# Kernel optimization log

Hardware: AMD Instinct MI355X
Metric: run time of the kernel (lower is better)

## Reference

```python
import jax, jax.numpy as jnp
import numpy as np

COMMITMENT_COST = 0.25
NUM_EMBEDDINGS = 8192
EMBEDDING_DIM = 256
N_TOKENS = 32768


def setup_inputs() -> dict:
    key = jax.random.key(0)
    k1, k2 = jax.random.split(key)
    inputs = jax.random.normal(k1, (N_TOKENS, EMBEDDING_DIM), dtype=jnp.float32)
    embed = jax.random.normal(k2, (EMBEDDING_DIM, NUM_EMBEDDINGS), dtype=jnp.float32)
    return {"inputs": inputs, "embed": embed}


def reference(inputs, embed):
    # inputs: [N, D], embed: [D, K]
    input_shape = inputs.shape
    flat = inputs.reshape(-1, embed.shape[0])
    input_norm = jnp.sum(flat * flat, axis=1, keepdims=True)
    embed_norm = jnp.sum(embed * embed, axis=0, keepdims=True)
    distances = input_norm + embed_norm - 2.0 * (flat @ embed)
    encoding_indices = jnp.argmin(distances, axis=1)  # [N]
    # direct gather instead of one-hot matmul (same math)
    quantized = jnp.take(embed.T, encoding_indices, axis=0).reshape(input_shape)
    e_latent_loss = jnp.mean((jax.lax.stop_gradient(quantized) - inputs) ** 2)
    loss = COMMITMENT_COST * e_latent_loss
    # straight-through estimator
    quantized_st = inputs + jax.lax.stop_gradient(quantized - inputs)
    return quantized_st, loss, encoding_indices
```

## Files before the change

### kernel.cpp

```cpp
#include <hip/hip_runtime.h>

#define N_TOK 32768
#define DIM   256
#define NEMB  8192

#define MARGIN_A  0.2f
#define MARGIN_T2 0.008f
#define MARGIN_B  0.0625f
#define GROUP 8
#define KSPLIT 4

typedef _Float16 f16;
typedef __attribute__((ext_vector_type(4))) _Float16 f16x4;
typedef __attribute__((ext_vector_type(8))) _Float16 f16x8;
typedef __attribute__((ext_vector_type(4))) float     f32x4;

__global__ void enorm_kernel(const float* __restrict__ E, float* __restrict__ enorm) {
    int k = blockIdx.x * blockDim.x + threadIdx.x;
    float s = 0.f;
#pragma unroll 8
    for (int d = 0; d < DIM; ++d) {
        float e = E[d * NEMB + k];
        s = fmaf(e, e, s);
    }
    enorm[k] = s;
}

__global__ __launch_bounds__(256) void cvt3_kernel(const float* __restrict__ E,
                                                   f16* __restrict__ ET,
                                                   f16* __restrict__ ETlo,
                                                   float* __restrict__ ET32,
                                                   int wlo, int wf32) {
    __shared__ float shf[64][65];
    const int tid = threadIdx.x;
    const int k0 = (blockIdx.x & 127) * 64;
    const int d0 = (blockIdx.x >> 7) * 64;
#pragma unroll
    for (int i = 0; i < 16; ++i) {
        int flat = i * 256 + tid;
        int k = flat & 63, d = flat >> 6;
        shf[k][d] = E[(size_t)(d0 + d) * NEMB + k0 + k];
    }
    __syncthreads();
#pragma unroll
    for (int i = 0; i < 16; ++i) {
        int flat = i * 256 + tid;
        int d = flat & 63, kk = flat >> 6;
        float v = shf[kk][d];
        f16 hi = (f16)v;
        ET[(size_t)(k0 + kk) * DIM + d0 + d] = hi;
        if (wlo)  ETlo[(size_t)(k0 + kk) * DIM + d0 + d] = (f16)(v - (float)hi);
        if (wf32) ET32[(size_t)(k0 + kk) * DIM + d0 + d] = v;
    }
}

__device__ __forceinline__ void gload_lds16(const void* g, void* l) {
    __builtin_amdgcn_global_load_lds(
        (const __attribute__((address_space(1))) unsigned int*)g,
        (__attribute__((address_space(3))) unsigned int*)l, 16, 0, 0);
}

__global__ __launch_bounds__(512, 2) void argmin_f16v8_kernel(
        const float* __restrict__ X, const f16* __restrict__ ET,
        const float* __restrict__ enorm,
        int* __restrict__ idx1o, int* __restrict__ idx2o, int* __restrict__ flago) {
    __shared__ char smem[65536];

    const int tid = threadIdx.x;
    const int w   = tid >> 6;
    const int l   = tid & 63;
    const int l15 = l & 15, l4 = l >> 4;
    const int h   = w & 1;
    const int cs  = w >> 1;
    const int r0  = blockIdx.x * 128;

    {
        const float4* X4 = (const float4*)(X + (size_t)r0 * DIM);
        f16* xs = (f16*)smem;
#pragma unroll
        for (int i = 0; i < 16; ++i) {
            int flat4 = tid + i * 512;
            float4 v = X4[flat4];
            int row = flat4 >> 6, d4 = flat4 & 63;
            f16x4 p = {(f16)v.x, (f16)v.y, (f16)v.z, (f16)v.w};
            *(f16x4*)(xs + row * 256 + d4 * 4) = p;
        }
    }
    __syncthreads();

    f16x8 Afr[4][8];
    {
        const f16* xs = (const f16*)smem;
#pragma unroll
        for (int mt = 0; mt < 4; ++mt)
#pragma unroll
            for (int c = 0; c < 8; ++c)
                Afr[mt][c] = *(const f16x8*)(xs + (h * 64 + mt * 16 + l15) * 256 + c * 32 + l4 * 8);
    }
    __syncthreads();

    float m1v[4][4], m2v[4][4];
    int   i1v[4][4];
#pragma unroll
    for (int mt = 0; mt < 4; ++mt)
#pragma unroll
        for (int rg = 0; rg < 4; ++rg) {
            m1v[mt][rg] = 3.4e38f; m2v[mt][rg] = 3.4e38f; i1v[mt][rg] = 0x7fffffff;
        }

    auto stage = [&](int kt, int buf) {
#pragma unroll
        for (int j = 0; j < 4; ++j) {
            const int code = w * 8 + j * 2 + (l >> 5);
            const f16* src = ET + ((size_t)kt * 64 + code) * 256
                               + (((l & 31) ^ (code & 7)) << 3);
            char* dst = smem + buf * 32768 + (w * 8 + j * 2) * 512;
            gload_lds16(src, dst);
        }
    };

    const int codeL = cs * 16 + l15;
    stage(0, 0);
    int p = 0;
    for (int kt = 0; kt < 128; ++kt) {
        __syncthreads();
        if (kt + 1 < 128) stage(kt + 1, p ^ 1);

        f32x4 acc[4];
#pragma unroll
        for (int mt = 0; mt < 4; ++mt) acc[mt] = (f32x4){0.f, 0.f, 0.f, 0.f};

        const f16* bb = (const f16*)(smem + p * 32768);
#pragma unroll
        for (int c = 0; c < 8; ++c) {
            const int g = (c * 4 + l4) ^ (l15 & 7);
            f16x8 b = *(const f16x8*)(bb + codeL * 256 + g * 8);
#pragma unroll
            for (int mt = 0; mt < 4; ++mt)
                acc[mt] = __builtin_amdgcn_mfma_f32_16x16x32_f16(Afr[mt][c], b, acc[mt], 0, 0, 0);
        }

        const int code = kt * 64 + codeL;
        const float en = enorm[code];
#pragma unroll
        for (int mt = 0; mt < 4; ++mt)
#pragma unroll
            for (int rg = 0; rg < 4; ++rg) {
                float v = fmaf(-2.f, acc[mt][rg], en);
                bool cl = v < m1v[mt][rg];
                m2v[mt][rg] = fminf(m2v[mt][rg], fmaxf(m1v[mt][rg], v));
                i1v[mt][rg] = cl ? code : i1v[mt][rg];
                m1v[mt][rg] = fminf(m1v[mt][rg], v);
            }
        p ^= 1;
    }

#pragma unroll
    for (int off = 1; off < 16; off <<= 1) {
#pragma unroll
        for (int mt = 0; mt < 4; ++mt)
#pragma unroll
            for (int rg = 0; rg < 4; ++rg) {
                float om1 = __shfl_xor(m1v[mt][rg], off);
                int   oi1 = __shfl_xor(i1v[mt][rg], off);
                float om2 = __shfl_xor(m2v[mt][rg], off);
                bool sw = (om1 < m1v[mt][rg]) ||
                          (om1 == m1v[mt][rg] && oi1 < i1v[mt][rg]);
                float hi = sw ? m1v[mt][rg] : om1;
                m1v[mt][rg] = sw ? om1 : m1v[mt][rg];
                i1v[mt][rg] = sw ? oi1 : i1v[mt][rg];
                m2v[mt][rg] = fminf(fminf(m2v[mt][rg], om2), hi);
            }
    }

    __syncthreads();
    float* sm1 = (float*)smem;
    int*   si1 = (int*)(smem + 2048);
    float* sm2 = (float*)(smem + 4096);
    if (l15 == 0) {
#pragma unroll
        for (int mt = 0; mt < 4; ++mt)
#pragma unroll
            for (int rg = 0; rg < 4; ++rg) {
                int row = h * 64 + mt * 16 + l4 * 4 + rg;
                sm1[row * 4 + cs] = m1v[mt][rg];
                si1[row * 4 + cs] = i1v[mt][rg];
                sm2[row * 4 + cs] = m2v[mt][rg];
            }
    }
    __syncthreads();
    if (tid < 128) {
        float M1 = 3.4e38f, M2 = 3.4e38f;
        int   I1 = 0x7fffffff;
#pragma unroll
        for (int e = 0; e < 4; ++e) {
            float v = sm1[tid * 4 + e]; int vi = si1[tid * 4 + e];
            if (v < M1 || (v == M1 && vi < I1)) { M2 = M1; M1 = v; I1 = vi; }
            else M2 = fminf(M2, v);
            M2 = fminf(M2, sm2[tid * 4 + e]);
        }
        int r = r0 + tid;
        idx1o[r] = I1;
        idx2o[r] = I1;
        flago[r] = (M2 - M1 < MARGIN_A) ? -1 : 0;
    }
}

__global__ __launch_bounds__(256) void compact_kernel(const int* __restrict__ flago,
        int* __restrict__ list, int* __restrict__ countp) {
    __shared__ int cnts[256], bases[256];
    const int tid = threadIdx.x;
    int c = 0;
    for (int i = 0; i < N_TOK / 256; ++i)
        c += (flago[tid * (N_TOK / 256) + i] < 0) ? 1 : 0;
    cnts[tid] = c;
    __syncthreads();
    if (tid == 0) {
        int run = 0;
        for (int t = 0; t < 256; ++t) { bases[t] = run; run += cnts[t]; }
        countp[0] = run;
    }
    __syncthreads();
    int o = bases[tid];
    for (int i = 0; i < N_TOK / 256; ++i) {
        int r = tid * (N_TOK / 256) + i;
        if (flago[r] < 0) list[o++] = r;
    }
}

__global__ __launch_bounds__(512) void rescan_split_kernel(
        const float* __restrict__ X, const f16* __restrict__ ET,
        const f16* __restrict__ ETlo, const float* __restrict__ enorm,
        const int* __restrict__ list, const int* __restrict__ countp,
        float* __restrict__ pm1, float* __restrict__ pm2, float* __restrict__ pm3,
        int* __restrict__ pi1, int* __restrict__ pi2) {
    __shared__ char smem[131072];
    const int cnt = countp[0];
    const int rb  = blockIdx.x >> 3;
    const int ks  = blockIdx.x & 7;
    if (rb * 64 >= cnt) return;

    const int tid = threadIdx.x, w = tid >> 6, l = tid & 63;
    const int l15 = l & 15, l4 = l >> 4;
    const int h = w & 1, cs = w >> 1;

    f16x8 Ah[2][8], Al[2][8];
#pragma unroll
    for (int mt = 0; mt < 2; ++mt) {
        int jg  = rb * 64 + h * 32 + mt * 16 + l15;
        int row = list[jg < cnt ? jg : cnt - 1];
        const float* xp = X + (size_t)row * DIM + l4 * 8;
#pragma unroll
        for (int c = 0; c < 8; ++c) {
            float4 v0 = *(const float4*)(xp + c * 32);
            float4 v1 = *(const float4*)(xp + c * 32 + 4);
            float xv[8] = {v0.x, v0.y, v0.z, v0.w, v1.x, v1.y, v1.z, v1.w};
            f16x8 hi, lo;
#pragma unroll
            for (int i = 0; i < 8; ++i) {
                f16 hv = (f16)xv[i];
                hi[i] = hv;
                lo[i] = (f16)(xv[i] - (float)hv);
            }
            Ah[mt][c] = hi; Al[mt][c] = lo;
        }
    }

    float m1v[2][4], m2v[2][4], m3v[2][4];
    int   i1v[2][4], i2v[2][4];
#pragma unroll
    for (int mt = 0; mt < 2; ++mt)
#pragma unroll
        for (int rg = 0; rg < 4; ++rg) {
            m1v[mt][rg] = 3.4e38f; m2v[mt][rg] = 3.4e38f; m3v[mt][rg] = 3.4e38f;
            i1v[mt][rg] = 0x7fffffff; i2v[mt][rg] = 0x7fffffff;
        }

    auto stage = [&](int kt, int buf) {
        const int tile = ks * 16 + kt;
#pragma unroll
        for (int j = 0; j < 4; ++j) {
            const int code = w * 8 + j * 2 + (l >> 5);
            size_t off = ((size_t)tile * 64 + code) * 256 + (((l & 31) ^ (code & 7)) << 3);
            char* dsth = smem + buf * 65536 + (w * 8 + j * 2) * 512;
            gload_lds16(ET + off, dsth);
            gload_lds16(ETlo + off, dsth + 32768);
        }
    };

    const int codeL = cs * 16 + l15;
    stage(0, 0);
    int p = 0;
    for (int kt = 0; kt < 16; ++kt) {
        __syncthreads();
        if (kt + 1 < 16) stage(kt + 1, p ^ 1);

        f32x4 acc[2];
#pragma unroll
        for (int mt = 0; mt < 2; ++mt) acc[mt] = (f32x4){0.f, 0.f, 0.f, 0.f};

        const f16* bh = (const f16*)(smem + p * 65536);
        const f16* bl = (const f16*)(smem + p * 65536 + 32768);
#pragma unroll
        for (int c = 0; c < 8; ++c) {
            const int g = (c * 4 + l4) ^ (l15 & 7);
            f16x8 vh = *(const f16x8*)(bh + codeL * 256 + g * 8);
            f16x8 vl = *(const f16x8*)(bl + codeL * 256 + g * 8);
#pragma unroll
            for (int mt = 0; mt < 2; ++mt) {
                acc[mt] = __builtin_amdgcn_mfma_f32_16x16x32_f16(Ah[mt][c], vh, acc[mt], 0, 0, 0);
                acc[mt] = __builtin_amdgcn_mfma_f32_16x16x32_f16(Ah[mt][c], vl, acc[mt], 0, 0, 0);
                acc[mt] = __builtin_amdgcn_mfma_f32_16x16x32_f16(Al[mt][c], vh, acc[mt], 0, 0, 0);
            }
        }

        const int code = (ks * 16 + kt) * 64 + codeL;
        const float en = enorm[code];
#pragma unroll
        for (int mt = 0; mt < 2; ++mt)
#pragma unroll
            for (int rg = 0; rg < 4; ++rg) {
                float v = fmaf(-2.f, acc[mt][rg], en);
                if (v < m1v[mt][rg]) {
                    m3v[mt][rg] = m2v[mt][rg];
                    m2v[mt][rg] = m1v[mt][rg]; i2v[mt][rg] = i1v[mt][rg];
                    m1v[mt][rg] = v;           i1v[mt][rg] = code;
                } else if (v < m2v[mt][rg]) {
                    m3v[mt][rg] = m2v[mt][rg];
                    m2v[mt][rg] = v;           i2v[mt][rg] = code;
                } else if (v < m3v[mt][rg]) {
                    m3v[mt][rg] = v;
                }
            }
        p ^= 1;
    }

    __syncthreads();
    float* Mm1 = (float*)smem;
    int*   Mi1 = (int*)(smem + 16384);
    float* Mm2 = (float*)(smem + 32768);
    int*   Mi2 = (int*)(smem + 49152);
    float* Mm3 = (float*)(smem + 65536);
#pragma unroll
    for (int mt = 0; mt < 2; ++mt)
#pragma unroll
        for (int rg = 0; rg < 4; ++rg) {
            int row = h * 32 + mt * 16 + l4 * 4 + rg;
            int e   = cs * 16 + l15;
            Mm1[row * 64 + e] = m1v[mt][rg];
            Mi1[row * 64 + e] = i1v[mt][rg];
            Mm2[row * 64 + e] = m2v[mt][rg];
            Mi2[row * 64 + e] = i2v[mt][rg];
            Mm3[row * 64 + e] = m3v[mt][rg];
        }
    __syncthreads();
    if (tid < 64) {
        float a1 = 3.4e38f, a2 = 3.4e38f, a3 = 3.4e38f;
        int   ai1 = 0x7fffffff, ai2 = 0x7fffffff;
        for (int e = 0; e < 64; ++e) {
            float b1 = Mm1[tid * 64 + e], b2 = Mm2[tid * 64 + e], b3 = Mm3[tid * 64 + e];
            int   bi1 = Mi1[tid * 64 + e], bi2 = Mi2[tid * 64 + e];
            if (b1 < a1 || (b1 == a1 && bi1 < ai1)) { a3 = a2; a2 = a1; ai2 = ai1; a1 = b1; ai1 = bi1; }
            else if (b1 < a2 || (b1 == a2 && bi1 < ai2)) { a3 = a2; a2 = b1; ai2 = bi1; }
            else if (b1 < a3) a3 = b1;
            if (b2 < a1 || (b2 == a1 && bi2 < ai1)) { a3 = a2; a2 = a1; ai2 = ai1; a1 = b2; ai1 = bi2; }
            else if (b2 < a2 || (b2 == a2 && bi2 < ai2)) { a3 = a2; a2 = b2; ai2 = bi2; }
            else if (b2 < a3) a3 = b2;
            if (b3 < a3) a3 = b3;
        }
        int jg = rb * 64 + tid;
        if (jg < cnt) {
            pm1[jg * 8 + ks] = a1; pm2[jg * 8 + ks] = a2; pm3[jg * 8 + ks] = a3;
            pi1[jg * 8 + ks] = ai1; pi2[jg * 8 + ks] = ai2;
        }
    }
}

__global__ void merge3_kernel(const int* __restrict__ list, const int* __restrict__ countp,
        const float* __restrict__ pm1, const float* __restrict__ pm2,
        const float* __restrict__ pm3,
        const int* __restrict__ pi1, const int* __restrict__ pi2,
        int* __restrict__ idx1o, int* __restrict__ idx2o, int* __restrict__ flago) {
    const int gid = blockIdx.x * 256 + threadIdx.x;
    if (gid >= countp[0]) return;
    float a1 = 3.4e38f, a2 = 3.4e38f, a3 = 3.4e38f;
    int   ai1 = 0x7fffffff, ai2 = 0x7fffffff;
#pragma unroll
    for (int ks = 0; ks < 8; ++ks) {
        float b1 = pm1[gid * 8 + ks], b2 = pm2[gid * 8 + ks], b3 = pm3[gid * 8 + ks];
        int   bi1 = pi1[gid * 8 + ks], bi2 = pi2[gid * 8 + ks];
        if (b1 < a1 || (b1 == a1 && bi1 < ai1)) { a3 = a2; a2 = a1; ai2 = ai1; a1 = b1; ai1 = bi1; }
        else if (b1 < a2 || (b1 == a2 && bi1 < ai2)) { a3 = a2; a2 = b1; ai2 = bi1; }
        else if (b1 < a3) a3 = b1;
        if (b2 < a1 || (b2 == a1 && bi2 < ai1)) { a3 = a2; a2 = a1; ai2 = ai1; a1 = b2; ai1 = bi2; }
        else if (b2 < a2 || (b2 == a2 && bi2 < ai2)) { a3 = a2; a2 = b2; ai2 = bi2; }
        else if (b2 < a3) a3 = b2;
        if (b3 < a3) a3 = b3;
    }
    const int row = list[gid];
    int fl = 0;
    if (a2 - a1 < MARGIN_T2) fl = (a3 - a1 < MARGIN_T2) ? 2 : 1;
    idx1o[row] = ai1; idx2o[row] = ai2; flago[row] = fl;
}

__global__ __launch_bounds__(256) void rescan_group_kernel(
        const float* __restrict__ X, const float* __restrict__ E,
        const float* __restrict__ enorm,
        const int* __restrict__ list, const int* __restrict__ countp,
        float* __restrict__ pm1, float* __restrict__ pm2, float* __restrict__ pm3,
        int* __restrict__ pi1, int* __restrict__ pi2) {
    const int cnt = countp[0];
    const int rc  = blockIdx.x >> 2;
    const int ks  = blockIdx.x & 3;
    if (rc * GROUP >= cnt) return;
    const int tid = threadIdx.x;
    __shared__ int rows_s[GROUP];
    __shared__ float sm1[256], sm2[256], sm3[256];
    __shared__ int   si1[256], si2[256];
    if (tid < GROUP) {
        int j = rc * GROUP + tid;
        rows_s[tid] = list[j < cnt ? j : cnt - 1];
    }
    __syncthreads();
    int rowsg[GROUP];
#pragma unroll
    for (int rr = 0; rr < GROUP; ++rr)
        rowsg[rr] = __builtin_amdgcn_readfirstlane(rows_s[rr]);

    float m1[GROUP], m2[GROUP], m3[GROUP];
    int   i1[GROUP], i2[GROUP];
#pragma unroll
    for (int rr = 0; rr < GROUP; ++rr) {
        m1[rr] = 3.4e38f; m2[rr] = 3.4e38f; m3[rr] = 3.4e38f;
        i1[rr] = 0x7fffffff; i2[rr] = 0x7fffffff;
    }
    for (int j = 0; j < 8; ++j) {
        const int k = ks * 2048 + j * 256 + tid;
        float acc[GROUP];
#pragma unroll
        for (int rr = 0; rr < GROUP; ++rr) acc[rr] = 0.f;
#pragma unroll 1
        for (int dc = 0; dc < 8; ++dc) {
            float ev[32];
#pragma unroll
            for (int i = 0; i < 32; ++i) ev[i] = E[(size_t)(dc * 32 + i) * NEMB + k];
#pragma unroll
            for (int rr = 0; rr < GROUP; ++rr) {
                const float* xp = X + (size_t)rowsg[rr] * DIM + dc * 32;
#pragma unroll
                for (int i = 0; i < 32; ++i) acc[rr] = fmaf(ev[i], xp[i], acc[rr]);
            }
        }
        const float en = enorm[k];
#pragma unroll
        for (int rr = 0; rr < GROUP; ++rr) {
            float v = fmaf(-2.f, acc[rr], en);
            if (v < m1[rr])      { m3[rr] = m2[rr]; m2[rr] = m1[rr]; i2[rr] = i1[rr]; m1[rr] = v; i1[rr] = k; }
            else if (v < m2[rr]) { m3[rr] = m2[rr]; m2[rr] = v; i2[rr] = k; }
            else if (v < m3[rr]) { m3[rr] = v; }
        }
    }
#pragma unroll 1
    for (int rr = 0; rr < GROUP; ++rr) {
        sm1[tid] = m1[rr]; sm2[tid] = m2[rr]; sm3[tid] = m3[rr];
        si1[tid] = i1[rr]; si2[tid] = i2[rr];
        __syncthreads();
        for (int st = 128; st > 0; st >>= 1) {
            if (tid < st) {
                float a1 = sm1[tid], a2 = sm2[tid], a3 = sm3[tid];
                int   ai1 = si1[tid], ai2 = si2[tid];
                float b1 = sm1[tid + st], b2 = sm2[tid + st], b3 = sm3[tid + st];
                int   bi1 = si1[tid + st], bi2 = si2[tid + st];
                if (b1 < a1 || (b1 == a1 && bi1 < ai1)) { a3 = a2; a2 = a1; ai2 = ai1; a1 = b1; ai1 = bi1; }
                else if (b1 < a2 || (b1 == a2 && bi1 < ai2)) { a3 = a2; a2 = b1; ai2 = bi1; }
                else if (b1 < a3) a3 = b1;
                if (b2 < a1 || (b2 == a1 && bi2 < ai1)) { a3 = a2; a2 = a1; ai2 = ai1; a1 = b2; ai1 = bi2; }
                else if (b2 < a2 || (b2 == a2 && bi2 < ai2)) { a3 = a2; a2 = b2; ai2 = bi2; }
                else if (b2 < a3) a3 = b2;
                if (b3 < a3) a3 = b3;
                sm1[tid] = a1; sm2[tid] = a2; sm3[tid] = a3; si1[tid] = ai1; si2[tid] = ai2;
            }
            __syncthreads();
        }
        if (tid == 0) {
            int jg = rc * GROUP + rr;
            if (jg < cnt) {
                pm1[jg * KSPLIT + ks] = sm1[0]; pm2[jg * KSPLIT + ks] = sm2[0];
                pm3[jg * KSPLIT + ks] = sm3[0];
                pi1[jg * KSPLIT + ks] = si1[0]; pi2[jg * KSPLIT + ks] = si2[0];
            }
        }
        __syncthreads();
    }
}

__global__ void merge_kernel(const int* __restrict__ list, const int* __restrict__ countp,
        const float* __restrict__ pm1, const float* __restrict__ pm2,
        const float* __restrict__ pm3,
        const int* __restrict__ pi1, const int* __restrict__ pi2,
        int* __restrict__ idx1o, int* __restrict__ idx2o, int* __restrict__ flago) {
    const int gid = blockIdx.x * 256 + threadIdx.x;
    if (gid >= countp[0]) return;
    float a1 = 3.4e38f, a2 = 3.4e38f, a3 = 3.4e38f;
    int   ai1 = 0x7fffffff, ai2 = 0x7fffffff;
#pragma unroll
    for (int ks = 0; ks < KSPLIT; ++ks) {
        float b1 = pm1[gid * KSPLIT + ks], b2 = pm2[gid * KSPLIT + ks], b3 = pm3[gid * KSPLIT + ks];
        int   bi1 = pi1[gid * KSPLIT + ks], bi2 = pi2[gid * KSPLIT + ks];
        if (b1 < a1 || (b1 == a1 && bi1 < ai1)) { a3 = a2; a2 = a1; ai2 = ai1; a1 = b1; ai1 = bi1; }
        else if (b1 < a2 || (b1 == a2 && bi1 < ai2)) { a3 = a2; a2 = b1; ai2 = bi1; }
        else if (b1 < a3) a3 = b1;
        if (b2 < a1 || (b2 == a1 && bi2 < ai1)) { a3 = a2; a2 = a1; ai2 = ai1; a1 = b2; ai1 = bi2; }
        else if (b2 < a2 || (b2 == a2 && bi2 < ai2)) { a3 = a2; a2 = b2; ai2 = bi2; }
        else if (b2 < a3) a3 = b2;
        if (b3 < a3) a3 = b3;
    }
    const int row = list[gid];
    int fl = 0;
    if (a2 - a1 < MARGIN_B) fl = (a3 - a1 < MARGIN_B) ? 2 : 1;
    idx1o[row] = ai1; idx2o[row] = ai2; flago[row] = fl;
}

#define BM 64
#define BN 128
#define DC 32
#define TM 4
#define TN 8
__global__ __launch_bounds__(256, 2) void argmin_f32_kernel(
        const float* __restrict__ X, const float* __restrict__ E,
        const float* __restrict__ enorm,
        int* __restrict__ idx1o, int* __restrict__ idx2o, int* __restrict__ flago) {
    __shared__ float As[DIM * BM];
    __shared__ float Bs[DC * BN];
    const int tid = threadIdx.x;
    const int r0  = blockIdx.x * BM;
    {
        const float4* X4 = (const float4*)(X + (size_t)r0 * DIM);
#pragma unroll
        for (int i = 0; i < 16; ++i) {
            int flat = tid + i * 256;
            int row = flat >> 6, c4 = flat & 63;
            float4 v = X4[flat];
            int d = c4 * 4;
            As[(d + 0) * BM + row] = v.x;
            As[(d + 1) * BM + row] = v.y;
            As[(d + 2) * BM + row] = v.z;
            As[(d + 3) * BM + row] = v.w;
        }
    }
    const int tc = tid & 15;
    const int tr = tid >> 4;
    float m1[TM], m2[TM], m3[TM];
    int   i1[TM], i2[TM];
#pragma unroll
    for (int j = 0; j < TM; ++j) { m1[j] = m2[j] = m3[j] = 3.4e38f; i1[j] = i2[j] = 0x7fffffff; }
    for (int kt = 0; kt < NEMB; kt += BN) {
        float acc[TM][TN];
#pragma unroll
        for (int j = 0; j < TM; ++j)
#pragma unroll
            for (int i = 0; i < TN; ++i) acc[j][i] = 0.f;
        for (int dc = 0; dc < DIM; dc += DC) {
            __syncthreads();
            const float4* E4 = (const float4*)E;
#pragma unroll
            for (int i = 0; i < 4; ++i) {
                int flat = tid + i * 256;
                int dd = flat >> 5, k4 = flat & 31;
                float4 v = E4[(size_t)(dc + dd) * (NEMB / 4) + (kt >> 2) + k4];
                *(float4*)&Bs[dd * BN + k4 * 4] = v;
            }
            __syncthreads();
#pragma unroll
            for (int dd = 0; dd < DC; ++dd) {
                float4 av = *(const float4*)&As[(dc + dd) * BM + tr * TM];
                float4 b0 = *(const float4*)&Bs[dd * BN + tc * TN];
                float4 b1 = *(const float4*)&Bs[dd * BN + tc * TN + 4];
                float a[TM] = {av.x, av.y, av.z, av.w};
                float b[TN] = {b0.x, b0.y, b0.z, b0.w, b1.x, b1.y, b1.z, b1.w};
#pragma unroll
                for (int j = 0; j < TM; ++j)
#pragma unroll
                    for (int i = 0; i < TN; ++i)
                        acc[j][i] = fmaf(a[j], b[i], acc[j][i]);
            }
        }
        float4 e0 = *(const float4*)&enorm[kt + tc * TN];
        float4 e1 = *(const float4*)&enorm[kt + tc * TN + 4];
        float en[TN] = {e0.x, e0.y, e0.z, e0.w, e1.x, e1.y, e1.z, e1.w};
#pragma unroll
        for (int j = 0; j < TM; ++j) {
#pragma unroll
            for (int i = 0; i < TN; ++i) {
                float v = en[i] - 2.f * acc[j][i];
                int k = kt + tc * TN + i;
                if (v < m1[j]) { m3[j] = m2[j]; m2[j] = m1[j]; i2[j] = i1[j]; m1[j] = v; i1[j] = k; }
                else if (v < m2[j]) { m3[j] = m2[j]; m2[j] = v; i2[j] = k; }
                else if (v < m3[j]) { m3[j] = v; }
            }
        }
    }
    __syncthreads();
    float* Mm1 = As;
    float* Mm2 = As + 1024;
    float* Mm3 = As + 2048;
    int*   Mi1 = (int*)(As + 3072);
    int*   Mi2 = (int*)(As + 4096);
#pragma unroll
    for (int j = 0; j < TM; ++j) {
        int row = tr * TM + j;
        Mm1[row * 16 + tc] = m1[j];
        Mm2[row * 16 + tc] = m2[j];
        Mm3[row * 16 + tc] = m3[j];
        Mi1[row * 16 + tc] = i1[j];
        Mi2[row * 16 + tc] = i2[j];
    }
    __syncthreads();
    if (tid < BM) {
        float M1 = 3.4e38f, M2 = 3.4e38f, M3 = 3.4e38f;
        int I1 = 0x7fffffff, I2 = 0x7fffffff;
        for (int e = 0; e < 16; ++e) {
            float v = Mm1[tid * 16 + e]; int vi = Mi1[tid * 16 + e];
            if (v < M1 || (v == M1 && vi < I1)) { M3 = M2; M2 = M1; I2 = I1; M1 = v; I1 = vi; }
            else if (v < M2 || (v == M2 && vi < I2)) { M3 = M2; M2 = v; I2 = vi; }
            else if (v < M3) { M3 = v; }
            v = Mm2[tid * 16 + e]; vi = Mi2[tid * 16 + e];
            if (v < M1 || (v == M1 && vi < I1)) { M3 = M2; M2 = M1; I2 = I1; M1 = v; I1 = vi; }
            else if (v < M2 || (v == M2 && vi < I2)) { M3 = M2; M2 = v; I2 = vi; }
            else if (v < M3) { M3 = v; }
            v = Mm3[tid * 16 + e];
            if (v < M3) M3 = v;
        }
        int r = r0 + tid;
        int fl = 0;
        if (M2 - M1 < MARGIN_B) fl = (M3 - M1 < MARGIN_B) ? 2 : 1;
        idx1o[r] = I1; idx2o[r] = I2; flago[r] = fl;
    }
}

__global__ __launch_bounds__(256) void refine_kernel(
        const float* __restrict__ X, const float* __restrict__ E,
        int* __restrict__ idx1o, const int* __restrict__ idx2o,
        const int* __restrict__ flago) {
    __shared__ double redA[256];
    __shared__ double redB[256];
    __shared__ int    redI[256];
    const int tid = threadIdx.x;
    for (int rr = 0; rr < 8; ++rr) {
        int r = blockIdx.x * 8 + rr;
        int flag = flago[r];
        if (flag == 0) continue;
        if (flag == 1) {
            int a = idx1o[r], b = idx2o[r];
            double x  = (double)X[(size_t)r * DIM + tid];
            double ea = (double)E[(size_t)tid * NEMB + a];
            double eb = (double)E[(size_t)tid * NEMB + b];
            redA[tid] = ea * (ea - 2.0 * x);
            redB[tid] = eb * (eb - 2.0 * x);
            __syncthreads();
            for (int s = 128; s > 0; s >>= 1) {
                if (tid < s) { redA[tid] += redA[tid + s]; redB[tid] += redB[tid + s]; }
                __syncthreads();
            }
            if (tid == 0) {
                double sa = redA[0], sb = redB[0];
                idx1o[r] = (sb < sa || (sb == sa && b < a)) ? b : a;
            }
            __syncthreads();
        } else {
            double bm = 1e300; int bi = 0x7fffffff;
            for (int k = tid; k < NEMB; k += 256) {
                double s = 0.0;
                for (int d = 0; d < DIM; ++d) {
                    double e = (double)E[(size_t)d * NEMB + k];
                    double x = (double)X[(size_t)r * DIM + d];
                    s += e * (e - 2.0 * x);
                }
                if (s < bm) { bm = s; bi = k; }
            }
            redA[tid] = bm; redI[tid] = bi;
            __syncthreads();
            for (int s = 128; s > 0; s >>= 1) {
                if (tid < s) {
                    if (redA[tid + s] < redA[tid] ||
                        (redA[tid + s] == redA[tid] && redI[tid + s] < redI[tid])) {
                        redA[tid] = redA[tid + s]; redI[tid] = redI[tid + s];
                    }
                }
                __syncthreads();
            }
            if (tid == 0) idx1o[r] = redI[0];
            __syncthreads();
        }
    }
}

__global__ __launch_bounds__(256) void gather_kernel(
        const float* __restrict__ X, const float* __restrict__ E,
        const int* __restrict__ idx,
        float* __restrict__ outq, float* __restrict__ outidxf,
        double* __restrict__ partials) {
    __shared__ double red[256];
    const int tid = threadIdx.x;
    const int row = blockIdx.x * 4 + (tid >> 6);
    const int d0  = (tid & 63) * 4;
    const int k   = idx[row];
    float4 x = *(const float4*)&X[(size_t)row * DIM + d0];
    float q0 = E[(size_t)(d0 + 0) * NEMB + k];
    float q1 = E[(size_t)(d0 + 1) * NEMB + k];
    float q2 = E[(size_t)(d0 + 2) * NEMB + k];
    float q3 = E[(size_t)(d0 + 3) * NEMB + k];
    float4 q = {q0, q1, q2, q3};
    *(float4*)&outq[(size_t)row * DIM + d0] = q;
    if ((tid & 63) == 0) outidxf[row] = (float)k;
    double s = 0.0, t;
    t = (double)q0 - (double)x.x; s += t * t;
    t = (double)q1 - (double)x.y; s += t * t;
    t = (double)q2 - (double)x.z; s += t * t;
    t = (double)q3 - (double)x.w; s += t * t;
    red[tid] = s;
    __syncthreads();
    for (int st = 128; st > 0; st >>= 1) {
        if (tid < st) red[tid] += red[tid + st];
        __syncthreads();
    }
    if (tid == 0) partials[blockIdx.x] = red[0];
}

__global__ __launch_bounds__(256) void gather2_kernel(
        const float* __restrict__ X, const float* __restrict__ ET32,
        const int* __restrict__ idx,
        float* __restrict__ outq, float* __restrict__ outidxf,
        double* __restrict__ partials) {
    __shared__ double red[256];
    const int tid = threadIdx.x;
    const int row = blockIdx.x * 4 + (tid >> 6);
    const int d0  = (tid & 63) * 4;
    const int k   = idx[row];
    float4 x = *(const float4*)&X[(size_t)row * DIM + d0];
    float4 q = *(const float4*)&ET32[(size_t)k * DIM + d0];
    *(float4*)&outq[(size_t)row * DIM + d0] = q;
    if ((tid & 63) == 0) outidxf[row] = (float)k;
    double s = 0.0, t;
    t = (double)q.x - (double)x.x; s += t * t;
    t = (double)q.y - (double)x.y; s += t * t;
    t = (double)q.z - (double)x.z; s += t * t;
    t = (double)q.w - (double)x.w; s += t * t;
    red[tid] = s;
    __syncthreads();
    for (int st = 128; st > 0; st >>= 1) {
        if (tid < st) red[tid] += red[tid + st];
        __syncthreads();
    }
    if (tid == 0) partials[blockIdx.x] = red[0];
}

__global__ __launch_bounds__(256) void loss_kernel(const double* __restrict__ partials,
                                                   float* __restrict__ outloss) {
    __shared__ double red[256];
    const int tid = threadIdx.x;
    double s = 0.0;
    for (int i = tid; i < N_TOK / 4; i += 256) s += partials[i];
    red[tid] = s;
    __syncthreads();
    for (int st = 128; st > 0; st >>= 1) {
        if (tid < st) red[tid] += red[tid + st];
        __syncthreads();
    }
    if (tid == 0)
        outloss[0] = (float)(0.25 * red[0] / (double)((size_t)N_TOK * DIM));
}

extern "C" void kernel_launch(void* const* d_in, const int* in_sizes, int n_in,
                              void* d_out, int out_size, void* d_ws, size_t ws_size,
                              hipStream_t stream) {
    const float* X = (const float*)d_in[0];
    const float* E = (const float*)d_in[1];

    float* outq    = (float*)d_out;
    float* outloss = outq + (size_t)N_TOK * DIM;
    float* outidx  = outloss + 1;

    char* base = (char*)d_ws;
    float*  enorm    = (float*)base;
    int*    idx1     = (int*)(base + 32768);
    int*    idx2     = (int*)(base + 163840);
    int*    flag     = (int*)(base + 294912);
    double* partials = (double*)(base + 425984);
    f16*    ET       = (f16*)(base + 524288);
    char*   etbase   = base + 524288;
    int*    listB    = (int*)etbase;
    int*    countB   = (int*)(etbase + 131072);
    float*  pm1B     = (float*)(etbase + 132096);
    float*  pm2B     = (float*)(etbase + 132096 + 524288);
    float*  pm3B     = (float*)(etbase + 132096 + 1048576);
    int*    pi1B     = (int*)  (etbase + 132096 + 1572864);
    int*    pi2B     = (int*)  (etbase + 132096 + 2097152);
    f16*    ETlo     = (f16*)(base + 4718592);
    int*    listA    = (int*)(base + 8912896);
    int*    countA   = (int*)(base + 9043968);
    float*  ET32     = (float*)(base + 9044992);
    float*  pm1A     = outq;
    float*  pm2A     = outq + 262144;
    float*  pm3A     = outq + 524288;
    int*    pi1A     = (int*)(outq + 786432);
    int*    pi2A     = (int*)(outq + 1048576);
    const size_t NEED_B  = 4718592;
    const size_t NEED_A  = 12190720;
    const size_t NEED_A2 = 9044992 + (size_t)NEMB * DIM * sizeof(float);

    enorm_kernel<<<NEMB / 256, 256, 0, stream>>>(E, enorm);
    if (ws_size >= NEED_A) {
        const int wf32 = (ws_size >= NEED_A2) ? 1 : 0;
        cvt3_kernel        <<<512,        256, 0, stream>>>(E, ET, ETlo, ET32, 1, wf32);
        argmin_f16v8_kernel<<<N_TOK / 128, 512, 0, stream>>>(X, ET, enorm, idx1, idx2, flag);
        compact_kernel     <<<1,          256, 0, stream>>>(flag, listA, countA);
        rescan_split_kernel<<<512 * 8,    512, 0, stream>>>(X, ET, ETlo, enorm, listA, countA,
                                                            pm1A, pm2A, pm3A, pi1A, pi2A);
        merge3_kernel      <<<N_TOK / 256, 256, 0, stream>>>(listA, countA, pm1A, pm2A, pm3A,
                                                             pi1A, pi2A, idx1, idx2, flag);
        refine_kernel<<<N_TOK / 8, 256, 0, stream>>>(X, E, idx1, idx2, flag);
        if (wf32)
            gather2_kernel<<<N_TOK / 4, 256, 0, stream>>>(X, ET32, idx1, outq, outidx, partials);
        else
            gather_kernel <<<N_TOK / 4, 256, 0, stream>>>(X, E, idx1, outq, outidx, partials);
    } else if (ws_size >= NEED_B) {
        cvt3_kernel        <<<512,        256, 0, stream>>>(E, ET, ET, (float*)ET, 0, 0);
        argmin_f16v8_kernel<<<N_TOK / 128, 512, 0, stream>>>(X, ET, enorm, idx1, idx2, flag);
        compact_kernel     <<<1,          256, 0, stream>>>(flag, listB, countB);
        rescan_group_kernel<<<(N_TOK / GROUP) * KSPLIT, 256, 0, stream>>>(X, E, enorm, listB, countB,
                                                                          pm1B, pm2B, pm3B, pi1B, pi2B);
        merge_kernel       <<<N_TOK / 256, 256, 0, stream>>>(listB, countB, pm1B, pm2B, pm3B,
                                                             pi1B, pi2B, idx1, idx2, flag);
        refine_kernel<<<N_TOK / 8, 256, 0, stream>>>(X, E, idx1, idx2, flag);
        gather_kernel<<<N_TOK / 4, 256, 0, stream>>>(X, E, idx1, outq, outidx, partials);
    } else {
        argmin_f32_kernel  <<<N_TOK / BM, 256, 0, stream>>>(X, E, enorm, idx1, idx2, flag);
        refine_kernel<<<N_TOK / 8, 256, 0, stream>>>(X, E, idx1, idx2, flag);
        gather_kernel<<<N_TOK / 4, 256, 0, stream>>>(X, E, idx1, outq, outidx, partials);
    }
    loss_kernel  <<<1,         256, 0, stream>>>(partials, outloss);
}
```

Baseline: 299.0 us.

## Triple-buffer argmin codebook tiles, cache enorm in LDS, fuse compaction via atomics

```diff
diff --git a/kernel.cpp b/kernel.cpp
--- a/kernel.cpp
+++ b/kernel.cpp
@@ -30,9 +30,11 @@
                                                    f16* __restrict__ ET,
                                                    f16* __restrict__ ETlo,
                                                    float* __restrict__ ET32,
+                                                   int* __restrict__ countz,
                                                    int wlo, int wf32) {
     __shared__ float shf[64][65];
     const int tid = threadIdx.x;
+    if (blockIdx.x == 0 && tid == 0) countz[0] = 0;
     const int k0 = (blockIdx.x & 127) * 64;
     const int d0 = (blockIdx.x >> 7) * 64;
 #pragma unroll
@@ -60,11 +62,12 @@
         (__attribute__((address_space(3))) unsigned int*)l, 16, 0, 0);
 }
 
-__global__ __launch_bounds__(512, 2) void argmin_f16v8_kernel(
+__global__ __launch_bounds__(512, 2) void argmin_f16v10_kernel(
         const float* __restrict__ X, const f16* __restrict__ ET,
         const float* __restrict__ enorm,
-        int* __restrict__ idx1o, int* __restrict__ idx2o, int* __restrict__ flago) {
-    __shared__ char smem[65536];
+        int* __restrict__ idx1o, int* __restrict__ idx2o, int* __restrict__ flago,
+        int* __restrict__ list, int* __restrict__ countp) {
+    __shared__ char smem[131072];
 
     const int tid = threadIdx.x;
     const int w   = tid >> 6;
@@ -75,6 +78,13 @@
     const int r0  = blockIdx.x * 128;
 
     {
+        float4* en4 = (float4*)(smem + 98304);
+        const float4* E4 = (const float4*)enorm;
+#pragma unroll
+        for (int i = 0; i < 4; ++i) en4[tid + i * 512] = E4[tid + i * 512];
+    }
+
+    {
         const float4* X4 = (const float4*)(X + (size_t)r0 * DIM);
         f16* xs = (f16*)smem;
 #pragma unroll
@@ -108,40 +118,35 @@
             m1v[mt][rg] = 3.4e38f; m2v[mt][rg] = 3.4e38f; i1v[mt][rg] = 0x7fffffff;
         }
 
-    auto stage = [&](int kt, int buf) {
+    auto stage = [&](int kt, int b) {
 #pragma unroll
         for (int j = 0; j < 4; ++j) {
             const int code = w * 8 + j * 2 + (l >> 5);
             const f16* src = ET + ((size_t)kt * 64 + code) * 256
                                + (((l & 31) ^ (code & 7)) << 3);
-            char* dst = smem + buf * 32768 + (w * 8 + j * 2) * 512;
+            char* dst = smem + b * 32768 + (w * 8 + j * 2) * 512;
             gload_lds16(src, dst);
         }
     };
 
     const int codeL = cs * 16 + l15;
-    stage(0, 0);
-    int p = 0;
-    for (int kt = 0; kt < 128; ++kt) {
-        __syncthreads();
-        if (kt + 1 < 128) stage(kt + 1, p ^ 1);
-
+    const float* enlds = (const float*)(smem + 98304);
+
+    auto compute = [&](int kt, int b) {
         f32x4 acc[4];
 #pragma unroll
         for (int mt = 0; mt < 4; ++mt) acc[mt] = (f32x4){0.f, 0.f, 0.f, 0.f};
-
-        const f16* bb = (const f16*)(smem + p * 32768);
+        const f16* bb = (const f16*)(smem + b * 32768);
 #pragma unroll
         for (int c = 0; c < 8; ++c) {
             const int g = (c * 4 + l4) ^ (l15 & 7);
-            f16x8 b = *(const f16x8*)(bb + codeL * 256 + g * 8);
+            f16x8 bfr = *(const f16x8*)(bb + codeL * 256 + g * 8);
 #pragma unroll
             for (int mt = 0; mt < 4; ++mt)
-                acc[mt] = __builtin_amdgcn_mfma_f32_16x16x32_f16(Afr[mt][c], b, acc[mt], 0, 0, 0);
-        }
-
+                acc[mt] = __builtin_amdgcn_mfma_f32_16x16x32_f16(Afr[mt][c], bfr, acc[mt], 0, 0, 0);
+        }
         const int code = kt * 64 + codeL;
-        const float en = enorm[code];
+        const float en = enlds[kt * 64 + codeL];
 #pragma unroll
         for (int mt = 0; mt < 4; ++mt)
 #pragma unroll
@@ -152,8 +157,27 @@
                 i1v[mt][rg] = cl ? code : i1v[mt][rg];
                 m1v[mt][rg] = fminf(m1v[mt][rg], v);
             }
-        p ^= 1;
-    }
+    };
+
+    stage(0, 0); stage(1, 1); stage(2, 2);
+
+    int b = 0;
+    for (int kt = 0; kt < 126; ++kt) {
+        asm volatile("s_waitcnt vmcnt(8)" ::: "memory");
+        __builtin_amdgcn_s_barrier();
+        compute(kt, b);
+        asm volatile("s_waitcnt lgkmcnt(0)" ::: "memory");
+        __builtin_amdgcn_s_barrier();
+        if (kt + 3 < 128) stage(kt + 3, b);
+        b = (b == 2) ? 0 : b + 1;
+    }
+    asm volatile("s_waitcnt vmcnt(4)" ::: "memory");
+    __builtin_amdgcn_s_barrier();
+    compute(126, b);
+    b = (b == 2) ? 0 : b + 1;
+    asm volatile("s_waitcnt vmcnt(0)" ::: "memory");
+    __builtin_amdgcn_s_barrier();
+    compute(127, b);
 
 #pragma unroll
     for (int off = 1; off < 16; off <<= 1) {
@@ -200,9 +224,19 @@
             M2 = fminf(M2, sm2[tid * 4 + e]);
         }
         int r = r0 + tid;
+        bool pred = (M2 - M1 < MARGIN_A);
         idx1o[r] = I1;
         idx2o[r] = I1;
-        flago[r] = (M2 - M1 < MARGIN_A) ? -1 : 0;
+        flago[r] = pred ? -1 : 0;
+        unsigned long long mask = __ballot(pred);
+        int lane = tid & 63;
+        int base = 0;
+        if (lane == 0) base = atomicAdd(countp, (int)__popcll(mask));
+        base = __shfl(base, 0);
+        if (pred) {
+            int off = (int)__popcll(mask & ((1ull << lane) - 1ull));
+            list[base + off] = r;
+        }
     }
 }
 
@@ -812,30 +846,31 @@
     enorm_kernel<<<NEMB / 256, 256, 0, stream>>>(E, enorm);
     if (ws_size >= NEED_A) {
         const int wf32 = (ws_size >= NEED_A2) ? 1 : 0;
-        cvt3_kernel        <<<512,        256, 0, stream>>>(E, ET, ETlo, ET32, 1, wf32);
-        argmin_f16v8_kernel<<<N_TOK / 128, 512, 0, stream>>>(X, ET, enorm, idx1, idx2, flag);
-        compact_kernel     <<<1,          256, 0, stream>>>(flag, listA, countA);
-        rescan_split_kernel<<<512 * 8,    512, 0, stream>>>(X, ET, ETlo, enorm, listA, countA,
-                                                            pm1A, pm2A, pm3A, pi1A, pi2A);
-        merge3_kernel      <<<N_TOK / 256, 256, 0, stream>>>(listA, countA, pm1A, pm2A, pm3A,
-                                                             pi1A, pi2A, idx1, idx2, flag);
+        cvt3_kernel         <<<512,        256, 0, stream>>>(E, ET, ETlo, ET32, countA, 1, wf32);
+        argmin_f16v10_kernel<<<N_TOK / 128, 512, 0, stream>>>(X, ET, enorm, idx1, idx2, flag,
+                                                              listA, countA);
+        rescan_split_kernel <<<512 * 8,    512, 0, stream>>>(X, ET, ETlo, enorm, listA, countA,
+                                                             pm1A, pm2A, pm3A, pi1A, pi2A);
+        merge3_kernel       <<<N_TOK / 256, 256, 0, stream>>>(listA, countA, pm1A, pm2A, pm3A,
+                                                              pi1A, pi2A, idx1, idx2, flag);
         refine_kernel<<<N_TOK / 8, 256, 0, stream>>>(X, E, idx1, idx2, flag);
         if (wf32)
             gather2_kernel<<<N_TOK / 4, 256, 0, stream>>>(X, ET32, idx1, outq, outidx, partials);
         else
             gather_kernel <<<N_TOK / 4, 256, 0, stream>>>(X, E, idx1, outq, outidx, partials);
     } else if (ws_size >= NEED_B) {
-        cvt3_kernel        <<<512,        256, 0, stream>>>(E, ET, ET, (float*)ET, 0, 0);
-        argmin_f16v8_kernel<<<N_TOK / 128, 512, 0, stream>>>(X, ET, enorm, idx1, idx2, flag);
-        compact_kernel     <<<1,          256, 0, stream>>>(flag, listB, countB);
-        rescan_group_kernel<<<(N_TOK / GROUP) * KSPLIT, 256, 0, stream>>>(X, E, enorm, listB, countB,
-                                                                          pm1B, pm2B, pm3B, pi1B, pi2B);
-        merge_kernel       <<<N_TOK / 256, 256, 0, stream>>>(listB, countB, pm1B, pm2B, pm3B,
-                                                             pi1B, pi2B, idx1, idx2, flag);
+        cvt3_kernel         <<<512,        256, 0, stream>>>(E, ET, ET, (float*)ET, countB, 0, 0);
+        argmin_f16v10_kernel<<<N_TOK / 128, 512, 0, stream>>>(X, ET, enorm, idx1, idx2, flag,
+                                                              listB, countB);
+        compact_kernel      <<<1,          256, 0, stream>>>(flag, listB, countB);
+        rescan_group_kernel <<<(N_TOK / GROUP) * KSPLIT, 256, 0, stream>>>(X, E, enorm, listB, countB,
+                                                                           pm1B, pm2B, pm3B, pi1B, pi2B);
+        merge_kernel        <<<N_TOK / 256, 256, 0, stream>>>(listB, countB, pm1B, pm2B, pm3B,
+                                                              pi1B, pi2B, idx1, idx2, flag);
         refine_kernel<<<N_TOK / 8, 256, 0, stream>>>(X, E, idx1, idx2, flag);
         gather_kernel<<<N_TOK / 4, 256, 0, stream>>>(X, E, idx1, outq, outidx, partials);
     } else {
-        argmin_f32_kernel  <<<N_TOK / BM, 256, 0, stream>>>(X, E, enorm, idx1, idx2, flag);
+        argmin_f32_kernel   <<<N_TOK / BM, 256, 0, stream>>>(X, E, enorm, idx1, idx2, flag);
         refine_kernel<<<N_TOK / 8, 256, 0, stream>>>(X, E, idx1, idx2, flag);
         gather_kernel<<<N_TOK / 4, 256, 0, stream>>>(X, E, idx1, outq, outidx, partials);
     }
```

Result: faster. 281.1 us (-6.0%).
